# Optimization experiments

Measured on AMD Instinct MI355X. Metric: run time of the kernel, lower is better.

## Reference

```python
import jax, jax.numpy as jnp
import numpy as np

N_NODES = 100_000
N_EDGES = 3_200_000  # avg in-degree 32
N_CLASSES = 16
TEMP = 0.5


def setup_inputs() -> dict:
    key = jax.random.key(0)
    k1, k2, k3 = jax.random.split(key, 3)
    src = jax.random.randint(k1, (N_EDGES,), 0, N_NODES, dtype=jnp.int32)
    # guarantee every node has at least one incoming edge so scatter-mean
    # and the sharpening normalization are well-defined
    dst = jnp.concatenate([
        jnp.arange(N_NODES, dtype=jnp.int32),
        jax.random.randint(k2, (N_EDGES - N_NODES,), 0, N_NODES, dtype=jnp.int32),
    ])
    edge_index = jnp.stack([src, dst], axis=0)  # [2, E]
    # positive predictions (log is taken downstream)
    aug_pred = jax.random.uniform(k3, (N_NODES, N_CLASSES), jnp.float32, 1e-3, 1.0)
    return {"edge_index": edge_index, "aug_pred": aug_pred}


def reference(edge_index, aug_pred):
    src = edge_index[0]  # message source nodes
    dst = edge_index[1]  # aggregation targets
    E = edge_index.shape[1]

    # scatter-mean aggregation: avg_pred[i] = mean_{e: dst[e]=i} aug_pred[src[e]]
    msg = aug_pred[src]                                   # [E, C]
    sums = jax.ops.segment_sum(msg, dst, num_segments=N_NODES)
    cnt = jax.ops.segment_sum(jnp.ones((E,), aug_pred.dtype), dst,
                              num_segments=N_NODES)
    avg_pred = sums / jnp.maximum(cnt, 1.0)[:, None]      # [N, C]

    # temperature sharpening + normalize
    p = avg_pred ** (1.0 / TEMP)
    sharp_avg_pred = p / jnp.sum(p, axis=1, keepdims=True)

    # edge-indexed gathers; dst side is detached in the original
    s = (avg_pred + 1e-10)[src]                            # [E, C]
    d = jax.lax.stop_gradient(sharp_avg_pred + 1e-10)[dst]  # [E, C]

    cr_loss = (d * jnp.log(d) - d * jnp.log(s)).sum(axis=1)  # [E]
    return cr_loss.mean()
```

## Files before the change

kernel.cpp:

```cpp
#include <hip/hip_runtime.h>

#define NCLS 16
#define NB 391
#define BSH 8
#define TILE 4096
#define BTHR 512
#define KPT 8
#define CAP 10240
#define ACAP 10

static __device__ __forceinline__ float bflo(unsigned u) {
  return __uint_as_float(u << 16);
}
static __device__ __forceinline__ float bfhi(unsigned u) {
  return __uint_as_float(u & 0xFFFF0000u);
}
static __device__ __forceinline__ unsigned f2bf1(float f) {
  unsigned u = __float_as_uint(f);
  return (u + 0x7FFF + ((u >> 16) & 1)) >> 16;
}
static __device__ __forceinline__ unsigned packbf(float a, float b) {
  return f2bf1(a) | (f2bf1(b) << 16);
}

__global__ void __launch_bounds__(BTHR) bin_kernel(const int* __restrict__ srcv,
                                                   const int* __restrict__ dstv,
                                                   const float2* __restrict__ aug,
                                                   unsigned* __restrict__ augh,
                                                   int* __restrict__ gcur,
                                                   int* __restrict__ packed,
                                                   int E, int n2) {
  __shared__ int hist[NB];
  __shared__ int off[NB];
  __shared__ int delta[NB];
  __shared__ int part[16];
  __shared__ int2 stag[TILE];
  int tid = threadIdx.x;
  for (int i = blockIdx.x * BTHR + tid; i < n2; i += gridDim.x * BTHR) {
    float2 v = aug[i];
    augh[i] = packbf(v.x, v.y);
  }
  int base = blockIdx.x * TILE;
  int cnt = min(TILE, E - base);
  for (int t = tid; t < NB; t += BTHR) hist[t] = 0;
  __syncthreads();
  int myw[KPT];
  int myp[KPT];
#pragma unroll
  for (int k = 0; k < KPT; k++) {
    int idx = tid + k * BTHR;
    myw[k] = -1;
    myp[k] = 0;
    if (idx < cnt) {
      int s = srcv[base + idx], d = dstv[base + idx];
      int b = d >> BSH;
      int r = atomicAdd(&hist[b], 1);
      myw[k] = s | ((d & 255) << 17);
      myp[k] = (b << 12) | r;
    }
  }
  __syncthreads();
  if (tid < 16) {
    int s = 0;
    int lo = tid * 25, hiX = min(NB, lo + 25);
    for (int j = lo; j < hiX; j++) { int v = hist[j]; off[j] = s; s += v; }
    part[tid] = s;
  }
  __syncthreads();
  if (tid == 0) {
    int run = 0;
    for (int j = 0; j < 16; j++) { int v = part[j]; part[j] = run; run += v; }
  }
  __syncthreads();
  for (int t = tid; t < NB; t += BTHR) off[t] += part[t / 25];
  __syncthreads();
  for (int t = tid; t < NB; t += BTHR) {
    int c = hist[t];
    int gb = c ? atomicAdd(&gcur[t], c) : 0;
    delta[t] = t * CAP + gb - off[t];
  }
  __syncthreads();
#pragma unroll
  for (int k = 0; k < KPT; k++) {
    if (myw[k] >= 0) {
      int b = myp[k] >> 12, r = myp[k] & 4095;
      int p = off[b] + r;
      int2 w;
      w.x = myw[k];
      w.y = p + delta[b];
      stag[p] = w;
    }
  }
  __syncthreads();
  for (int i = tid; i < cnt; i += BTHR) {
    int2 w = stag[i];
    packed[w.y] = w.x;
  }
}

__global__ void __launch_bounds__(1024) agg_kernel(const int* __restrict__ gcur,
                                                   const int* __restrict__ packed,
                                                   const unsigned* __restrict__ augh,
                                                   unsigned* __restrict__ logs,
                                                   float* __restrict__ dvec,
                                                   double* __restrict__ acc, int N) {
  __shared__ int ssrc[CAP];
  __shared__ int hist[256];
  __shared__ int off[256];
  __shared__ float red[16];
  int tid = threadIdx.x;
  int b = blockIdx.x;
  int rbeg = b * CAP;
  int cnt = gcur[b];
  if (tid < 256) hist[tid] = 0;
  __syncthreads();
  int myw[ACAP];
  int myr[ACAP];
#pragma unroll
  for (int k = 0; k < ACAP; k++) {
    int i = tid + k * 1024;
    int w = (i < cnt) ? packed[rbeg + i] : -1;
    myw[k] = w;
    myr[k] = (w >= 0) ? atomicAdd(&hist[w >> 17], 1) : 0;
  }
  __syncthreads();
  if (tid < 64) {
    int h0 = hist[4 * tid], h1 = hist[4 * tid + 1];
    int h2 = hist[4 * tid + 2], h3 = hist[4 * tid + 3];
    int tot = h0 + h1 + h2 + h3;
    int inc = tot;
#pragma unroll
    for (int o = 1; o < 64; o <<= 1) {
      int u = __shfl_up(inc, o, 64);
      if (tid >= o) inc += u;
    }
    int exc = inc - tot;
    off[4 * tid] = exc;
    off[4 * tid + 1] = exc + h0;
    off[4 * tid + 2] = exc + h0 + h1;
    off[4 * tid + 3] = exc + h0 + h1 + h2;
  }
  __syncthreads();
#pragma unroll
  for (int k = 0; k < ACAP; k++) {
    int w = myw[k];
    if (w >= 0) ssrc[off[w >> 17] + myr[k]] = w & 0x1FFFF;
  }
  __syncthreads();
  int node = tid >> 2, lane = tid & 3;
  int boff = off[node];
  int deg = hist[node];
  double s0 = 0., s1 = 0., s2 = 0., s3 = 0.;
  int wsh = lane << 1;
  int e = 0;
  for (; e + 8 <= deg; e += 8) {
    int q0 = ssrc[boff + e],     q1 = ssrc[boff + e + 1];
    int q2 = ssrc[boff + e + 2], q3 = ssrc[boff + e + 3];
    int q4 = ssrc[boff + e + 4], q5 = ssrc[boff + e + 5];
    int q6 = ssrc[boff + e + 6], q7 = ssrc[boff + e + 7];
    uint2 g0 = *reinterpret_cast<const uint2*>(augh + ((size_t)q0 << 3) + wsh);
    uint2 g1 = *reinterpret_cast<const uint2*>(augh + ((size_t)q1 << 3) + wsh);
    uint2 g2 = *reinterpret_cast<const uint2*>(augh + ((size_t)q2 << 3) + wsh);
    uint2 g3 = *reinterpret_cast<const uint2*>(augh + ((size_t)q3 << 3) + wsh);
    uint2 g4 = *reinterpret_cast<const uint2*>(augh + ((size_t)q4 << 3) + wsh);
    uint2 g5 = *reinterpret_cast<const uint2*>(augh + ((size_t)q5 << 3) + wsh);
    uint2 g6 = *reinterpret_cast<const uint2*>(augh + ((size_t)q6 << 3) + wsh);
    uint2 g7 = *reinterpret_cast<const uint2*>(augh + ((size_t)q7 << 3) + wsh);
    s0 += (double)bflo(g0.x) + (double)bflo(g1.x) + (double)bflo(g2.x) + (double)bflo(g3.x) +
          (double)bflo(g4.x) + (double)bflo(g5.x) + (double)bflo(g6.x) + (double)bflo(g7.x);
    s1 += (double)bfhi(g0.x) + (double)bfhi(g1.x) + (double)bfhi(g2.x) + (double)bfhi(g3.x) +
          (double)bfhi(g4.x) + (double)bfhi(g5.x) + (double)bfhi(g6.x) + (double)bfhi(g7.x);
    s2 += (double)bflo(g0.y) + (double)bflo(g1.y) + (double)bflo(g2.y) + (double)bflo(g3.y) +
          (double)bflo(g4.y) + (double)bflo(g5.y) + (double)bflo(g6.y) + (double)bflo(g7.y);
    s3 += (double)bfhi(g0.y) + (double)bfhi(g1.y) + (double)bfhi(g2.y) + (double)bfhi(g3.y) +
          (double)bfhi(g4.y) + (double)bfhi(g5.y) + (double)bfhi(g6.y) + (double)bfhi(g7.y);
  }
  for (; e < deg; e++) {
    int q0 = ssrc[boff + e];
    uint2 g0 = *reinterpret_cast<const uint2*>(augh + ((size_t)q0 << 3) + wsh);
    s0 += (double)bflo(g0.x); s1 += (double)bfhi(g0.x);
    s2 += (double)bflo(g0.y); s3 += (double)bfhi(g0.y);
  }
  double dinv = 1.0 / (double)(deg > 0 ? deg : 1);
  float a0 = (float)(s0 * dinv), a1 = (float)(s1 * dinv);
  float a2 = (float)(s2 * dinv), a3 = (float)(s3 * dinv);
  float p2 = a0 * a0 + a1 * a1 + a2 * a2 + a3 * a3;
  p2 += __shfl_xor(p2, 1, 64);
  p2 += __shfl_xor(p2, 2, 64);
  float ip = 1.0f / p2;
  float d0 = a0 * a0 * ip + 1e-10f, d1 = a1 * a1 * ip + 1e-10f;
  float d2 = a2 * a2 * ip + 1e-10f, d3 = a3 * a3 * ip + 1e-10f;
  float h = d0 * __logf(d0) + d1 * __logf(d1) + d2 * __logf(d2) + d3 * __logf(d3);
  h += __shfl_xor(h, 1, 64);
  h += __shfl_xor(h, 2, 64);
  int g = (b << BSH) + node;
  float contrib = 0.f;
  if (g < N) {
    uint2 lw;
    lw.x = packbf(__logf(a0 + 1e-10f), __logf(a1 + 1e-10f));
    lw.y = packbf(__logf(a2 + 1e-10f), __logf(a3 + 1e-10f));
    *reinterpret_cast<uint2*>(logs + ((size_t)g << 3) + wsh) = lw;
    float4 dd;
    dd.x = d0; dd.y = d1; dd.z = d2; dd.w = d3;
    *reinterpret_cast<float4*>(dvec + ((size_t)g << 4) + (lane << 2)) = dd;
    if (lane == 0) contrib = (float)deg * h;
  }
#pragma unroll
  for (int o = 32; o >= 1; o >>= 1) contrib += __shfl_xor(contrib, o, 64);
  if ((tid & 63) == 0) red[tid >> 6] = contrib;
  __syncthreads();
  if (tid == 0) {
    float s = 0.f;
#pragma unroll
    for (int wv = 0; wv < 16; wv++) s += red[wv];
    atomicAdd(acc, (double)s);
  }
}

#define ASTR 17
__global__ void __launch_bounds__(1024) loss_kernel(const int* __restrict__ gcur,
                                                    const int* __restrict__ packed,
                                                    const unsigned* __restrict__ logs,
                                                    const float* __restrict__ dvec,
                                                    double* __restrict__ acc,
                                                    int* __restrict__ done,
                                                    float* __restrict__ out,
                                                    int N, int E) {
  __shared__ float sdv[256 * ASTR];
  __shared__ double red[16];
  int tid = threadIdx.x;
  int b = blockIdx.x;
  int rbeg = b * CAP;
  int cnt = gcur[b];
  int rend = rbeg + cnt;
  int nb0 = b << BSH;
  {
    const float4* gsrc = reinterpret_cast<const float4*>(dvec + ((size_t)nb0 << 4));
    int nvalid = min(256, N - nb0);
    int nf4 = nvalid * 4;
    for (int i = tid; i < nf4; i += 1024) {
      float4 v = gsrc[i];
      float* r = sdv + (i >> 2) * ASTR + ((i & 3) << 2);
      r[0] = v.x; r[1] = v.y; r[2] = v.z; r[3] = v.w;
    }
  }
  __syncthreads();
  double dot = 0.0;
  int i = rbeg + tid;
  for (; i + 1024 < rend; i += 2048) {
    int wa = packed[i];
    int wb = packed[i + 1024];
    int sa = wa & 0x1FFFF, la = wa >> 17;
    int sb = wb & 0x1FFFF, lb = wb >> 17;
    const uint4* ga = reinterpret_cast<const uint4*>(logs + ((size_t)sa << 3));
    const uint4* gb = reinterpret_cast<const uint4*>(logs + ((size_t)sb << 3));
    uint4 a0 = ga[0], a1 = ga[1];
    uint4 b0 = gb[0], b1 = gb[1];
    const float* ra = sdv + la * ASTR;
    const float* rb = sdv + lb * ASTR;
    float ea = ra[0] * bflo(a0.x) + ra[1] * bfhi(a0.x) +
               ra[2] * bflo(a0.y) + ra[3] * bfhi(a0.y) +
               ra[4] * bflo(a0.z) + ra[5] * bfhi(a0.z) +
               ra[6] * bflo(a0.w) + ra[7] * bfhi(a0.w) +
               ra[8] * bflo(a1.x) + ra[9] * bfhi(a1.x) +
               ra[10] * bflo(a1.y) + ra[11] * bfhi(a1.y) +
               ra[12] * bflo(a1.z) + ra[13] * bfhi(a1.z) +
               ra[14] * bflo(a1.w) + ra[15] * bfhi(a1.w);
    float eb = rb[0] * bflo(b0.x) + rb[1] * bfhi(b0.x) +
               rb[2] * bflo(b0.y) + rb[3] * bfhi(b0.y) +
               rb[4] * bflo(b0.z) + rb[5] * bfhi(b0.z) +
               rb[6] * bflo(b0.w) + rb[7] * bfhi(b0.w) +
               rb[8] * bflo(b1.x) + rb[9] * bfhi(b1.x) +
               rb[10] * bflo(b1.y) + rb[11] * bfhi(b1.y) +
               rb[12] * bflo(b1.z) + rb[13] * bfhi(b1.z) +
               rb[14] * bflo(b1.w) + rb[15] * bfhi(b1.w);
    dot += (double)ea + (double)eb;
  }
  if (i < rend) {
    int wa = packed[i];
    int sa = wa & 0x1FFFF, la = wa >> 17;
    const uint4* ga = reinterpret_cast<const uint4*>(logs + ((size_t)sa << 3));
    uint4 a0 = ga[0], a1 = ga[1];
    const float* ra = sdv + la * ASTR;
    float ea = ra[0] * bflo(a0.x) + ra[1] * bfhi(a0.x) +
               ra[2] * bflo(a0.y) + ra[3] * bfhi(a0.y) +
               ra[4] * bflo(a0.z) + ra[5] * bfhi(a0.z) +
               ra[6] * bflo(a0.w) + ra[7] * bfhi(a0.w) +
               ra[8] * bflo(a1.x) + ra[9] * bfhi(a1.x) +
               ra[10] * bflo(a1.y) + ra[11] * bfhi(a1.y) +
               ra[12] * bflo(a1.z) + ra[13] * bfhi(a1.z) +
               ra[14] * bflo(a1.w) + ra[15] * bfhi(a1.w);
    dot += (double)ea;
  }
#pragma unroll
  for (int o = 32; o >= 1; o >>= 1) dot += __shfl_xor(dot, o, 64);
  if ((tid & 63) == 0) red[tid >> 6] = dot;
  __syncthreads();
  if (tid == 0) {
    double s = 0.0;
#pragma unroll
    for (int wv = 0; wv < 16; wv++) s += red[wv];
    atomicAdd(acc, -s);
    __threadfence();
    int t = atomicAdd(done, 1);
    if (t == (int)gridDim.x - 1) {
      double v = atomicAdd(acc, 0.0);
      out[0] = (float)(v / (double)E);
    }
  }
}

extern "C" void kernel_launch(void* const* d_in, const int* in_sizes, int n_in,
                              void* d_out, int out_size, void* d_ws, size_t ws_size,
                              hipStream_t stream) {
  const int* edge_index = (const int*)d_in[0];
  const float* aug_pred = (const float*)d_in[1];
  const int E = in_sizes[0] / 2;
  const int N = in_sizes[1] / NCLS;

  const int* srcv = edge_index;
  const int* dstv = edge_index + E;

  char* p = (char*)d_ws;
  auto alloc = [&](size_t bytes) {
    char* r = p;
    p += (bytes + 255) & ~(size_t)255;
    return r;
  };
  double* acc = (double*)alloc(8);
  int* done = (int*)alloc(4);
  int* gcur = (int*)alloc(NB * 4);
  int* packed = (int*)alloc((size_t)NB * CAP * 4);
  unsigned* augh = (unsigned*)alloc((size_t)N * NCLS * 2);
  unsigned* logs = (unsigned*)alloc((size_t)N * NCLS * 2);
  float* dvec = (float*)alloc((size_t)N * NCLS * 4);

  size_t zero_bytes = (size_t)((char*)packed - (char*)d_ws);
  hipMemsetAsync(d_ws, 0, zero_bytes, stream);

  int n2 = N * NCLS / 2;
  int tiles = (E + TILE - 1) / TILE;
  bin_kernel<<<tiles, BTHR, 0, stream>>>(srcv, dstv, (const float2*)aug_pred,
                                         augh, gcur, packed, E, n2);
  agg_kernel<<<NB, 1024, 0, stream>>>(gcur, packed, augh, logs, dvec, acc, N);
  loss_kernel<<<NB, 1024, 0, stream>>>(gcur, packed, logs, dvec, acc, done,
                                       (float*)d_out, N, E);
}
```

Measured before the change: 156.6 us.

## Fuse aggregation and loss kernels with a grid-wide barrier, keeping per-block data in LDS

Merges the aggregation and loss kernels into one persistent kernel of 512 threads per block. A spin-wait on a global counter serves as the grid barrier between the phases. The sorted edge list and the sharpened per-node distribution stay in shared memory, so the dvec round trip through global memory and the second read of packed are dropped. Each node now uses two threads with 16-byte gathers instead of four threads with 8-byte gathers. The spin barrier relies on all 391 blocks being co-resident; if they are not, the kernel deadlocks. The larger per-thread register arrays may also reduce occupancy.

Result: slower. 280.8 us (+79.3%).

```diff
diff --git a/kernel.cpp b/kernel.cpp
--- a/kernel.cpp
+++ b/kernel.cpp
@@ -7,7 +7,9 @@
 #define BTHR 512
 #define KPT 8
 #define CAP 10240
-#define ACAP 10
+#define FTHR 512
+#define ACAP 20
+#define ASTR 17
 
 static __device__ __forceinline__ float bflo(unsigned u) {
   return __uint_as_float(u << 16);
@@ -98,16 +100,21 @@
   }
 }
 
-__global__ void __launch_bounds__(1024) agg_kernel(const int* __restrict__ gcur,
-                                                   const int* __restrict__ packed,
-                                                   const unsigned* __restrict__ augh,
-                                                   unsigned* __restrict__ logs,
-                                                   float* __restrict__ dvec,
-                                                   double* __restrict__ acc, int N) {
+__global__ void __launch_bounds__(FTHR, 4) fused_kernel(const int* __restrict__ gcur,
+                                                        const int* __restrict__ packed,
+                                                        const unsigned* __restrict__ augh,
+                                                        unsigned* __restrict__ logs,
+                                                        double* __restrict__ acc,
+                                                        int* __restrict__ done,
+                                                        int* __restrict__ done2,
+                                                        float* __restrict__ out,
+                                                        int N, int E) {
   __shared__ int ssrc[CAP];
   __shared__ int hist[256];
   __shared__ int off[256];
-  __shared__ float red[16];
+  __shared__ float sdv[256 * ASTR];
+  __shared__ float redf[8];
+  __shared__ double redd[8];
   int tid = threadIdx.x;
   int b = blockIdx.x;
   int rbeg = b * CAP;
@@ -118,7 +125,7 @@
   int myr[ACAP];
 #pragma unroll
   for (int k = 0; k < ACAP; k++) {
-    int i = tid + k * 1024;
+    int i = tid + k * FTHR;
     int w = (i < cnt) ? packed[rbeg + i] : -1;
     myw[k] = w;
     myr[k] = (w >= 0) ? atomicAdd(&hist[w >> 17], 1) : 0;
@@ -144,168 +151,152 @@
 #pragma unroll
   for (int k = 0; k < ACAP; k++) {
     int w = myw[k];
-    if (w >= 0) ssrc[off[w >> 17] + myr[k]] = w & 0x1FFFF;
-  }
-  __syncthreads();
-  int node = tid >> 2, lane = tid & 3;
+    if (w >= 0) ssrc[off[w >> 17] + myr[k]] = w;
+  }
+  __syncthreads();
+  int node = tid >> 1, t8 = tid & 1;
   int boff = off[node];
   int deg = hist[node];
-  double s0 = 0., s1 = 0., s2 = 0., s3 = 0.;
-  int wsh = lane << 1;
-  int e = 0;
-  for (; e + 8 <= deg; e += 8) {
-    int q0 = ssrc[boff + e],     q1 = ssrc[boff + e + 1];
-    int q2 = ssrc[boff + e + 2], q3 = ssrc[boff + e + 3];
-    int q4 = ssrc[boff + e + 4], q5 = ssrc[boff + e + 5];
-    int q6 = ssrc[boff + e + 6], q7 = ssrc[boff + e + 7];
-    uint2 g0 = *reinterpret_cast<const uint2*>(augh + ((size_t)q0 << 3) + wsh);
-    uint2 g1 = *reinterpret_cast<const uint2*>(augh + ((size_t)q1 << 3) + wsh);
-    uint2 g2 = *reinterpret_cast<const uint2*>(augh + ((size_t)q2 << 3) + wsh);
-    uint2 g3 = *reinterpret_cast<const uint2*>(augh + ((size_t)q3 << 3) + wsh);
-    uint2 g4 = *reinterpret_cast<const uint2*>(augh + ((size_t)q4 << 3) + wsh);
-    uint2 g5 = *reinterpret_cast<const uint2*>(augh + ((size_t)q5 << 3) + wsh);
-    uint2 g6 = *reinterpret_cast<const uint2*>(augh + ((size_t)q6 << 3) + wsh);
-    uint2 g7 = *reinterpret_cast<const uint2*>(augh + ((size_t)q7 << 3) + wsh);
-    s0 += (double)bflo(g0.x) + (double)bflo(g1.x) + (double)bflo(g2.x) + (double)bflo(g3.x) +
-          (double)bflo(g4.x) + (double)bflo(g5.x) + (double)bflo(g6.x) + (double)bflo(g7.x);
-    s1 += (double)bfhi(g0.x) + (double)bfhi(g1.x) + (double)bfhi(g2.x) + (double)bfhi(g3.x) +
-          (double)bfhi(g4.x) + (double)bfhi(g5.x) + (double)bfhi(g6.x) + (double)bfhi(g7.x);
-    s2 += (double)bflo(g0.y) + (double)bflo(g1.y) + (double)bflo(g2.y) + (double)bflo(g3.y) +
-          (double)bflo(g4.y) + (double)bflo(g5.y) + (double)bflo(g6.y) + (double)bflo(g7.y);
-    s3 += (double)bfhi(g0.y) + (double)bfhi(g1.y) + (double)bfhi(g2.y) + (double)bfhi(g3.y) +
-          (double)bfhi(g4.y) + (double)bfhi(g5.y) + (double)bfhi(g6.y) + (double)bfhi(g7.y);
-  }
-  for (; e < deg; e++) {
-    int q0 = ssrc[boff + e];
-    uint2 g0 = *reinterpret_cast<const uint2*>(augh + ((size_t)q0 << 3) + wsh);
-    s0 += (double)bflo(g0.x); s1 += (double)bfhi(g0.x);
-    s2 += (double)bflo(g0.y); s3 += (double)bfhi(g0.y);
-  }
-  double dinv = 1.0 / (double)(deg > 0 ? deg : 1);
-  float a0 = (float)(s0 * dinv), a1 = (float)(s1 * dinv);
-  float a2 = (float)(s2 * dinv), a3 = (float)(s3 * dinv);
-  float p2 = a0 * a0 + a1 * a1 + a2 * a2 + a3 * a3;
-  p2 += __shfl_xor(p2, 1, 64);
-  p2 += __shfl_xor(p2, 2, 64);
-  float ip = 1.0f / p2;
-  float d0 = a0 * a0 * ip + 1e-10f, d1 = a1 * a1 * ip + 1e-10f;
-  float d2 = a2 * a2 * ip + 1e-10f, d3 = a3 * a3 * ip + 1e-10f;
-  float h = d0 * __logf(d0) + d1 * __logf(d1) + d2 * __logf(d2) + d3 * __logf(d3);
-  h += __shfl_xor(h, 1, 64);
-  h += __shfl_xor(h, 2, 64);
+  int woff = t8 << 2;
   int g = (b << BSH) + node;
-  float contrib = 0.f;
-  if (g < N) {
-    uint2 lw;
-    lw.x = packbf(__logf(a0 + 1e-10f), __logf(a1 + 1e-10f));
-    lw.y = packbf(__logf(a2 + 1e-10f), __logf(a3 + 1e-10f));
-    *reinterpret_cast<uint2*>(logs + ((size_t)g << 3) + wsh) = lw;
-    float4 dd;
-    dd.x = d0; dd.y = d1; dd.z = d2; dd.w = d3;
-    *reinterpret_cast<float4*>(dvec + ((size_t)g << 4) + (lane << 2)) = dd;
-    if (lane == 0) contrib = (float)deg * h;
-  }
-#pragma unroll
-  for (int o = 32; o >= 1; o >>= 1) contrib += __shfl_xor(contrib, o, 64);
-  if ((tid & 63) == 0) red[tid >> 6] = contrib;
+  {
+    double s0 = 0., s1 = 0., s2 = 0., s3 = 0., s4 = 0., s5 = 0., s6 = 0., s7 = 0.;
+    int e = 0;
+    for (; e + 4 <= deg; e += 4) {
+      int q0 = ssrc[boff + e] & 0x1FFFF,     q1 = ssrc[boff + e + 1] & 0x1FFFF;
+      int q2 = ssrc[boff + e + 2] & 0x1FFFF, q3 = ssrc[boff + e + 3] & 0x1FFFF;
+      uint4 g0 = *reinterpret_cast<const uint4*>(augh + ((size_t)q0 << 3) + woff);
+      uint4 g1 = *reinterpret_cast<const uint4*>(augh + ((size_t)q1 << 3) + woff);
+      uint4 g2 = *reinterpret_cast<const uint4*>(augh + ((size_t)q2 << 3) + woff);
+      uint4 g3 = *reinterpret_cast<const uint4*>(augh + ((size_t)q3 << 3) + woff);
+      s0 += (double)bflo(g0.x) + (double)bflo(g1.x) + (double)bflo(g2.x) + (double)bflo(g3.x);
+      s1 += (double)bfhi(g0.x) + (double)bfhi(g1.x) + (double)bfhi(g2.x) + (double)bfhi(g3.x);
+      s2 += (double)bflo(g0.y) + (double)bflo(g1.y) + (double)bflo(g2.y) + (double)bflo(g3.y);
+      s3 += (double)bfhi(g0.y) + (double)bfhi(g1.y) + (double)bfhi(g2.y) + (double)bfhi(g3.y);
+      s4 += (double)bflo(g0.z) + (double)bflo(g1.z) + (double)bflo(g2.z) + (double)bflo(g3.z);
+      s5 += (double)bfhi(g0.z) + (double)bfhi(g1.z) + (double)bfhi(g2.z) + (double)bfhi(g3.z);
+      s6 += (double)bflo(g0.w) + (double)bflo(g1.w) + (double)bflo(g2.w) + (double)bflo(g3.w);
+      s7 += (double)bfhi(g0.w) + (double)bfhi(g1.w) + (double)bfhi(g2.w) + (double)bfhi(g3.w);
+    }
+    for (; e < deg; e++) {
+      int q0 = ssrc[boff + e] & 0x1FFFF;
+      uint4 g0 = *reinterpret_cast<const uint4*>(augh + ((size_t)q0 << 3) + woff);
+      s0 += (double)bflo(g0.x); s1 += (double)bfhi(g0.x);
+      s2 += (double)bflo(g0.y); s3 += (double)bfhi(g0.y);
+      s4 += (double)bflo(g0.z); s5 += (double)bfhi(g0.z);
+      s6 += (double)bflo(g0.w); s7 += (double)bfhi(g0.w);
+    }
+    double dinv = 1.0 / (double)(deg > 0 ? deg : 1);
+    float a0 = (float)(s0 * dinv), a1 = (float)(s1 * dinv);
+    float a2 = (float)(s2 * dinv), a3 = (float)(s3 * dinv);
+    float a4 = (float)(s4 * dinv), a5 = (float)(s5 * dinv);
+    float a6 = (float)(s6 * dinv), a7 = (float)(s7 * dinv);
+    float p2 = a0 * a0 + a1 * a1 + a2 * a2 + a3 * a3 +
+               a4 * a4 + a5 * a5 + a6 * a6 + a7 * a7;
+    p2 += __shfl_xor(p2, 1, 64);
+    float ip = 1.0f / p2;
+    float d0 = a0 * a0 * ip + 1e-10f, d1 = a1 * a1 * ip + 1e-10f;
+    float d2 = a2 * a2 * ip + 1e-10f, d3 = a3 * a3 * ip + 1e-10f;
+    float d4 = a4 * a4 * ip + 1e-10f, d5 = a5 * a5 * ip + 1e-10f;
+    float d6 = a6 * a6 * ip + 1e-10f, d7 = a7 * a7 * ip + 1e-10f;
+    float h = d0 * __logf(d0) + d1 * __logf(d1) + d2 * __logf(d2) + d3 * __logf(d3) +
+              d4 * __logf(d4) + d5 * __logf(d5) + d6 * __logf(d6) + d7 * __logf(d7);
+    h += __shfl_xor(h, 1, 64);
+    float contrib = 0.f;
+    if (g < N) {
+      uint4 lw;
+      lw.x = packbf(__logf(a0 + 1e-10f), __logf(a1 + 1e-10f));
+      lw.y = packbf(__logf(a2 + 1e-10f), __logf(a3 + 1e-10f));
+      lw.z = packbf(__logf(a4 + 1e-10f), __logf(a5 + 1e-10f));
+      lw.w = packbf(__logf(a6 + 1e-10f), __logf(a7 + 1e-10f));
+      *reinterpret_cast<uint4*>(logs + ((size_t)g << 3) + woff) = lw;
+      float* sr = sdv + node * ASTR + (t8 << 3);
+      sr[0] = d0; sr[1] = d1; sr[2] = d2; sr[3] = d3;
+      sr[4] = d4; sr[5] = d5; sr[6] = d6; sr[7] = d7;
+      if (t8 == 0) contrib = (float)deg * h;
+    }
+#pragma unroll
+    for (int o = 32; o >= 1; o >>= 1) contrib += __shfl_xor(contrib, o, 64);
+    if ((tid & 63) == 0) redf[tid >> 6] = contrib;
+    __syncthreads();
+    if (tid == 0) {
+      float ss = 0.f;
+#pragma unroll
+      for (int wv = 0; wv < 8; wv++) ss += redf[wv];
+      atomicAdd(acc, (double)ss);
+    }
+  }
+  __threadfence();
   __syncthreads();
   if (tid == 0) {
-    float s = 0.f;
-#pragma unroll
-    for (int wv = 0; wv < 16; wv++) s += red[wv];
-    atomicAdd(acc, (double)s);
-  }
-}
-
-#define ASTR 17
-__global__ void __launch_bounds__(1024) loss_kernel(const int* __restrict__ gcur,
-                                                    const int* __restrict__ packed,
-                                                    const unsigned* __restrict__ logs,
-                                                    const float* __restrict__ dvec,
-                                                    double* __restrict__ acc,
-                                                    int* __restrict__ done,
-                                                    float* __restrict__ out,
-                                                    int N, int E) {
-  __shared__ float sdv[256 * ASTR];
-  __shared__ double red[16];
-  int tid = threadIdx.x;
-  int b = blockIdx.x;
-  int rbeg = b * CAP;
-  int cnt = gcur[b];
-  int rend = rbeg + cnt;
-  int nb0 = b << BSH;
+    atomicAdd(done, 1);
+    while (atomicAdd(done, 0) < NB) __builtin_amdgcn_s_sleep(8);
+  }
+  __syncthreads();
+  __threadfence();
   {
-    const float4* gsrc = reinterpret_cast<const float4*>(dvec + ((size_t)nb0 << 4));
-    int nvalid = min(256, N - nb0);
-    int nf4 = nvalid * 4;
-    for (int i = tid; i < nf4; i += 1024) {
-      float4 v = gsrc[i];
-      float* r = sdv + (i >> 2) * ASTR + ((i & 3) << 2);
-      r[0] = v.x; r[1] = v.y; r[2] = v.z; r[3] = v.w;
-    }
-  }
-  __syncthreads();
-  double dot = 0.0;
-  int i = rbeg + tid;
-  for (; i + 1024 < rend; i += 2048) {
-    int wa = packed[i];
-    int wb = packed[i + 1024];
-    int sa = wa & 0x1FFFF, la = wa >> 17;
-    int sb = wb & 0x1FFFF, lb = wb >> 17;
-    const uint4* ga = reinterpret_cast<const uint4*>(logs + ((size_t)sa << 3));
-    const uint4* gb = reinterpret_cast<const uint4*>(logs + ((size_t)sb << 3));
-    uint4 a0 = ga[0], a1 = ga[1];
-    uint4 b0 = gb[0], b1 = gb[1];
-    const float* ra = sdv + la * ASTR;
-    const float* rb = sdv + lb * ASTR;
-    float ea = ra[0] * bflo(a0.x) + ra[1] * bfhi(a0.x) +
-               ra[2] * bflo(a0.y) + ra[3] * bfhi(a0.y) +
-               ra[4] * bflo(a0.z) + ra[5] * bfhi(a0.z) +
-               ra[6] * bflo(a0.w) + ra[7] * bfhi(a0.w) +
-               ra[8] * bflo(a1.x) + ra[9] * bfhi(a1.x) +
-               ra[10] * bflo(a1.y) + ra[11] * bfhi(a1.y) +
-               ra[12] * bflo(a1.z) + ra[13] * bfhi(a1.z) +
-               ra[14] * bflo(a1.w) + ra[15] * bfhi(a1.w);
-    float eb = rb[0] * bflo(b0.x) + rb[1] * bfhi(b0.x) +
-               rb[2] * bflo(b0.y) + rb[3] * bfhi(b0.y) +
-               rb[4] * bflo(b0.z) + rb[5] * bfhi(b0.z) +
-               rb[6] * bflo(b0.w) + rb[7] * bfhi(b0.w) +
-               rb[8] * bflo(b1.x) + rb[9] * bfhi(b1.x) +
-               rb[10] * bflo(b1.y) + rb[11] * bfhi(b1.y) +
-               rb[12] * bflo(b1.z) + rb[13] * bfhi(b1.z) +
-               rb[14] * bflo(b1.w) + rb[15] * bfhi(b1.w);
-    dot += (double)ea + (double)eb;
-  }
-  if (i < rend) {
-    int wa = packed[i];
-    int sa = wa & 0x1FFFF, la = wa >> 17;
-    const uint4* ga = reinterpret_cast<const uint4*>(logs + ((size_t)sa << 3));
-    uint4 a0 = ga[0], a1 = ga[1];
-    const float* ra = sdv + la * ASTR;
-    float ea = ra[0] * bflo(a0.x) + ra[1] * bfhi(a0.x) +
-               ra[2] * bflo(a0.y) + ra[3] * bfhi(a0.y) +
-               ra[4] * bflo(a0.z) + ra[5] * bfhi(a0.z) +
-               ra[6] * bflo(a0.w) + ra[7] * bfhi(a0.w) +
-               ra[8] * bflo(a1.x) + ra[9] * bfhi(a1.x) +
-               ra[10] * bflo(a1.y) + ra[11] * bfhi(a1.y) +
-               ra[12] * bflo(a1.z) + ra[13] * bfhi(a1.z) +
-               ra[14] * bflo(a1.w) + ra[15] * bfhi(a1.w);
-    dot += (double)ea;
-  }
-#pragma unroll
-  for (int o = 32; o >= 1; o >>= 1) dot += __shfl_xor(dot, o, 64);
-  if ((tid & 63) == 0) red[tid >> 6] = dot;
-  __syncthreads();
-  if (tid == 0) {
-    double s = 0.0;
-#pragma unroll
-    for (int wv = 0; wv < 16; wv++) s += red[wv];
-    atomicAdd(acc, -s);
-    __threadfence();
-    int t = atomicAdd(done, 1);
-    if (t == (int)gridDim.x - 1) {
-      double v = atomicAdd(acc, 0.0);
-      out[0] = (float)(v / (double)E);
+    double dot = 0.0;
+    int i = tid;
+    for (; i + FTHR < cnt; i += 2 * FTHR) {
+      int wa = ssrc[i];
+      int wb = ssrc[i + FTHR];
+      int sa = wa & 0x1FFFF, la = wa >> 17;
+      int sb = wb & 0x1FFFF, lb = wb >> 17;
+      const uint4* ga = reinterpret_cast<const uint4*>(logs + ((size_t)sa << 3));
+      const uint4* gb = reinterpret_cast<const uint4*>(logs + ((size_t)sb << 3));
+      uint4 a0 = ga[0], a1 = ga[1];
+      uint4 b0 = gb[0], b1 = gb[1];
+      const float* ra = sdv + la * ASTR;
+      const float* rb = sdv + lb * ASTR;
+      float ea = ra[0] * bflo(a0.x) + ra[1] * bfhi(a0.x) +
+                 ra[2] * bflo(a0.y) + ra[3] * bfhi(a0.y) +
+                 ra[4] * bflo(a0.z) + ra[5] * bfhi(a0.z) +
+                 ra[6] * bflo(a0.w) + ra[7] * bfhi(a0.w) +
+                 ra[8] * bflo(a1.x) + ra[9] * bfhi(a1.x) +
+                 ra[10] * bflo(a1.y) + ra[11] * bfhi(a1.y) +
+                 ra[12] * bflo(a1.z) + ra[13] * bfhi(a1.z) +
+                 ra[14] * bflo(a1.w) + ra[15] * bfhi(a1.w);
+      float eb = rb[0] * bflo(b0.x) + rb[1] * bfhi(b0.x) +
+                 rb[2] * bflo(b0.y) + rb[3] * bfhi(b0.y) +
+                 rb[4] * bflo(b0.z) + rb[5] * bfhi(b0.z) +
+                 rb[6] * bflo(b0.w) + rb[7] * bfhi(b0.w) +
+                 rb[8] * bflo(b1.x) + rb[9] * bfhi(b1.x) +
+                 rb[10] * bflo(b1.y) + rb[11] * bfhi(b1.y) +
+                 rb[12] * bflo(b1.z) + rb[13] * bfhi(b1.z) +
+                 rb[14] * bflo(b1.w) + rb[15] * bfhi(b1.w);
+      dot += (double)ea + (double)eb;
+    }
+    if (i < cnt) {
+      int wa = ssrc[i];
+      int sa = wa & 0x1FFFF, la = wa >> 17;
+      const uint4* ga = reinterpret_cast<const uint4*>(logs + ((size_t)sa << 3));
+      uint4 a0 = ga[0], a1 = ga[1];
+      const float* ra = sdv + la * ASTR;
+      float ea = ra[0] * bflo(a0.x) + ra[1] * bfhi(a0.x) +
+                 ra[2] * bflo(a0.y) + ra[3] * bfhi(a0.y) +
+                 ra[4] * bflo(a0.z) + ra[5] * bfhi(a0.z) +
+                 ra[6] * bflo(a0.w) + ra[7] * bfhi(a0.w) +
+                 ra[8] * bflo(a1.x) + ra[9] * bfhi(a1.x) +
+                 ra[10] * bflo(a1.y) + ra[11] * bfhi(a1.y) +
+                 ra[12] * bflo(a1.z) + ra[13] * bfhi(a1.z) +
+                 ra[14] * bflo(a1.w) + ra[15] * bfhi(a1.w);
+      dot += (double)ea;
+    }
+#pragma unroll
+    for (int o = 32; o >= 1; o >>= 1) dot += __shfl_xor(dot, o, 64);
+    if ((tid & 63) == 0) redd[tid >> 6] = dot;
+    __syncthreads();
+    if (tid == 0) {
+      double ss = 0.0;
+#pragma unroll
+      for (int wv = 0; wv < 8; wv++) ss += redd[wv];
+      atomicAdd(acc, -ss);
+      __threadfence();
+      int t = atomicAdd(done2, 1);
+      if (t == (int)gridDim.x - 1) {
+        double v = atomicAdd(acc, 0.0);
+        out[0] = (float)(v / (double)E);
+      }
     }
   }
 }
@@ -329,11 +320,11 @@
   };
   double* acc = (double*)alloc(8);
   int* done = (int*)alloc(4);
+  int* done2 = (int*)alloc(4);
   int* gcur = (int*)alloc(NB * 4);
   int* packed = (int*)alloc((size_t)NB * CAP * 4);
   unsigned* augh = (unsigned*)alloc((size_t)N * NCLS * 2);
   unsigned* logs = (unsigned*)alloc((size_t)N * NCLS * 2);
-  float* dvec = (float*)alloc((size_t)N * NCLS * 4);
 
   size_t zero_bytes = (size_t)((char*)packed - (char*)d_ws);
   hipMemsetAsync(d_ws, 0, zero_bytes, stream);
@@ -342,7 +333,6 @@
   int tiles = (E + TILE - 1) / TILE;
   bin_kernel<<<tiles, BTHR, 0, stream>>>(srcv, dstv, (const float2*)aug_pred,
                                          augh, gcur, packed, E, n2);
-  agg_kernel<<<NB, 1024, 0, stream>>>(gcur, packed, augh, logs, dvec, acc, N);
-  loss_kernel<<<NB, 1024, 0, stream>>>(gcur, packed, logs, dvec, acc, done,
-                                       (float*)d_out, N, E);
-}
+  fused_kernel<<<NB, FTHR, 0, stream>>>(gcur, packed, augh, logs, acc, done, done2,
+                                        (float*)d_out, N, E);
+}
```
